# Kernel optimization log

Hardware: AMD Instinct MI355X
Metric: run time of the kernel (lower is better)

Reference implementation:

```python
import jax, jax.numpy as jnp
from jax import lax
import numpy as np

B, C0, C1 = 4, 128, 256
HF = WF = 256
HC = WC = 128
N_CROPS = 2048
WS0, WS1 = 8, 10
PAD0, PAD1 = 0, 1
STRIDE = 8
NW = (WF + 2 * PAD0 - WS0) // STRIDE + 1  # 32 windows per row (same for both crops)


def setup_inputs() -> dict:
    key = jax.random.key(0)
    ks = jax.random.split(key, 16)
    inp = {
        'x0_fine': jax.random.normal(ks[0], (B, C0, HF, WF), jnp.float32),
        'x0_coarse': jax.random.normal(ks[1], (B, C1, HC, WC), jnp.float32),
        'x1_fine': jax.random.normal(ks[2], (B, C0, HF, WF), jnp.float32),
        'x1_coarse': jax.random.normal(ks[3], (B, C1, HC, WC), jnp.float32),
        'proj0_w': jax.random.normal(ks[4], (C1, C0, 1, 1), jnp.float32) * 0.05,
        'proj_last_w': jax.random.normal(ks[5], (C1, C1, 1, 1), jnp.float32) * 0.05,
        'fuse_w1': jax.random.normal(ks[6], (C1, C1, 3, 3), jnp.float32) * 0.02,
        'bn_gamma': jnp.ones((C1,), jnp.float32),
        'bn_beta': jnp.zeros((C1,), jnp.float32),
        'bn_mean': jax.random.normal(ks[7], (C1,), jnp.float32) * 0.1,
        'bn_var': jax.random.uniform(ks[8], (C1,), jnp.float32) + 0.5,
        'fuse_w2': jax.random.normal(ks[9], (C0, C1, 3, 3), jnp.float32) * 0.02,
        'b_idx': jax.random.randint(ks[10], (N_CROPS,), 0, B, jnp.int32),
        'i_idx': jax.random.randint(ks[11], (N_CROPS,), 0, NW * NW, jnp.int32),
        'j_idx': jax.random.randint(ks[12], (N_CROPS,), 0, NW * NW, jnp.int32),
    }
    return inp


def conv2d(x, w, pad):
    return lax.conv_general_dilated(x, w, (1, 1), [(pad, pad), (pad, pad)],
                                    dimension_numbers=('NCHW', 'OIHW', 'NCHW'))


def up2_align_corners(x):
    # bilinear upsample x2 with align_corners=True, separable along H then W
    def interp(x, axis):
        n_in = x.shape[axis]
        n_out = 2 * n_in
        pos = jnp.arange(n_out, dtype=x.dtype) * ((n_in - 1) / (n_out - 1))
        i0 = jnp.clip(jnp.floor(pos).astype(jnp.int32), 0, n_in - 2)
        w = pos - i0.astype(x.dtype)
        a = jnp.take(x, i0, axis=axis)
        b = jnp.take(x, i0 + 1, axis=axis)
        shp = [1] * x.ndim
        shp[axis] = n_out
        w = w.reshape(shp)
        return a * (1 - w) + b * w
    return interp(interp(x, 2), 3)


def fuse(fine, coarse, proj0_w, proj_last_w, fuse_w1, bn_gamma, bn_beta, bn_mean, bn_var, fuse_w2):
    x0 = conv2d(coarse, proj_last_w, 0)                 # projs[-1]
    x0 = conv2d(fine, proj0_w, 0) + up2_align_corners(x0)
    y = conv2d(x0, fuse_w1, 1)
    inv = lax.rsqrt(bn_var + 1e-5)
    y = (y - bn_mean[None, :, None, None]) * (bn_gamma * inv)[None, :, None, None] + bn_beta[None, :, None, None]
    y = jnp.where(y >= 0, y, 0.01 * y)                  # LeakyReLU
    return conv2d(y, fuse_w2, 1)


def crop_windows(x, ws, pad, b, idx):
    # direct sparse window gather; avoids materializing the dense unfold tensor
    xp = jnp.pad(x, ((0, 0), (0, 0), (pad, pad), (pad, pad)))
    nW = (x.shape[3] + 2 * pad - ws) // STRIDE + 1
    r0 = (idx // nW) * STRIDE
    c0 = (idx % nW) * STRIDE
    rows = r0[:, None] + jnp.arange(ws)                 # [n, ws]
    cols = c0[:, None] + jnp.arange(ws)                 # [n, ws]
    crops = xp[b[:, None, None], :, rows[:, :, None], cols[:, None, :]]  # [n, ws, ws, C]
    return jnp.transpose(crops, (0, 3, 1, 2))           # [n, C, ws, ws]


def reference(x0_fine, x0_coarse, x1_fine, x1_coarse, proj0_w, proj_last_w,
              fuse_w1, bn_gamma, bn_beta, bn_mean, bn_var, fuse_w2,
              b_idx, i_idx, j_idx):
    # shapes equal -> concat, fuse once, chunk (matches torch branch)
    fine = jnp.concatenate([x0_fine, x1_fine], 0)
    coarse = jnp.concatenate([x0_coarse, x1_coarse], 0)
    y = fuse(fine, coarse, proj0_w, proj_last_w, fuse_w1, bn_gamma, bn_beta, bn_mean, bn_var, fuse_w2)
    x0, x1 = y[:B], y[B:]
    x0_cropped = crop_windows(x0, WS0, PAD0, b_idx, i_idx)
    x1_cropped = crop_windows(x1, WS1, PAD1, b_idx, j_idx)
    return (x0_cropped, x1_cropped)
```

## Files before the change

### kernel.cpp

```cpp
#include <hip/hip_runtime.h>

typedef __attribute__((ext_vector_type(8))) __bf16 bf16x8;
typedef __attribute__((ext_vector_type(4))) float f32x4;
typedef __attribute__((ext_vector_type(16))) float f32x16;

__device__ __forceinline__ unsigned short fbf(float f) {
  union { float f; unsigned u; } x; x.f = f;
  unsigned r = x.u + 0x7fffu + ((x.u >> 16) & 1u);
  return (unsigned short)(r >> 16);
}
__device__ __forceinline__ float bf2f(unsigned short h) {
  union { unsigned u; float f; } x; x.u = ((unsigned)h) << 16;
  return x.f;
}

#define OFF_WPL 0u
#define OFF_WP0 131072u
#define OFF_WT1 196608u
#define OFF_WT2 1376256u
#define OFF_BNS 1966080u
#define OFF_BNB 1967104u
#define OFF_T1  4194304u
#define OFF_X0  (OFF_T1 + 67108864u)
#define OFF_Y   (OFF_X0 + 268435456u)
#define OFF_YF  OFF_T1

__global__ void prep_kernel(const float* __restrict__ pl, const float* __restrict__ p0,
                            const float* __restrict__ w1, const float* __restrict__ w2,
                            const float* __restrict__ gam, const float* __restrict__ bet,
                            const float* __restrict__ mean, const float* __restrict__ var,
                            unsigned short* __restrict__ wpl, unsigned short* __restrict__ wp0,
                            unsigned short* __restrict__ wt1, unsigned short* __restrict__ wt2,
                            float* __restrict__ bns, float* __restrict__ bnb) {
  int t = blockIdx.x * blockDim.x + threadIdx.x;
  int stride = gridDim.x * blockDim.x;
  for (int i = t; i < 65536; i += stride) wpl[i] = fbf(pl[i]);
  for (int i = t; i < 32768; i += stride) wp0[i] = fbf(p0[i]);
  for (int i = t; i < 589824; i += stride) {
    int e = i & 7, l = (i >> 3) & 63, ks = (i >> 9) & 1;
    int cib = (i >> 10) & 7, cb = (i >> 13) & 7, tap = i >> 16;
    int ci = cib * 32 + ks * 16 + (l >> 5) * 8 + e;
    int co = cb * 32 + (l & 31);
    wt1[i] = fbf(w1[(co * 256 + ci) * 9 + tap]);
  }
  for (int i = t; i < 294912; i += stride) {
    int e = i & 7, l = (i >> 3) & 63, ks = (i >> 9) & 1;
    int cib = (i >> 10) & 7, cb = (i >> 13) & 3, tap = i >> 15;
    int ci = cib * 32 + ks * 16 + (l >> 5) * 8 + e;
    int co = cb * 32 + (l & 31);
    wt2[i] = fbf(w2[(co * 256 + ci) * 9 + tap]);
  }
  for (int i = t; i < 256; i += stride) {
    float s = gam[i] * rsqrtf(var[i] + 1e-5f);
    bns[i] = s; bnb[i] = bet[i] - mean[i] * s;
  }
}

template <int K, int HW, int WD, int EPI>
__global__ __launch_bounds__(512) void gemm1x1_kernel(
    const float* __restrict__ srcA, const float* __restrict__ srcB,
    const unsigned short* __restrict__ wmat,
    unsigned short* __restrict__ outp,
    const unsigned short* __restrict__ t1) {
  __shared__ unsigned short in_lds[128 * 32];
  __shared__ unsigned short w_lds[128 * 32];
  const int tid = threadIdx.x;
  const int pix0 = blockIdx.x * 128;
  const int co0 = blockIdx.y * 128;
  const int n = pix0 / HW;
  const int rem = pix0 % HW;
  const int h = rem / WD;
  const int w0 = rem % WD;
  const float* src = (n < 4) ? (srcA + (size_t)n * K * HW) : (srcB + (size_t)(n - 4) * K * HW);
  const float* rowbase = src + (size_t)h * WD + w0;
  const int wv = tid >> 6, lane = tid & 63;
  const int pw = wv >> 1, cw = wv & 1;
  const int l15 = lane & 15, k8 = lane >> 4;
  f32x4 zero = {0.f, 0.f, 0.f, 0.f};
  f32x4 acc[2][4];
#pragma unroll
  for (int i = 0; i < 2; i++)
#pragma unroll
    for (int j = 0; j < 4; j++) acc[i][j] = zero;
  const int sci = tid >> 4;
  const int sps = (tid & 15) * 8;
  const int wrow = tid >> 2, wsg = tid & 3;
  for (int cib = 0; cib < K / 32; ++cib) {
    int ci0 = cib * 32;
    __syncthreads();
    {
      const float* p = rowbase + (size_t)(ci0 + sci) * HW + sps;
      float4 v0 = *(const float4*)p;
      float4 v1 = *(const float4*)(p + 4);
      float vv[8] = {v0.x, v0.y, v0.z, v0.w, v1.x, v1.y, v1.z, v1.w};
#pragma unroll
      for (int i = 0; i < 8; i++) {
        int row = sps + i;
        int g = (sci >> 3) ^ ((row >> 1) & 3);
        in_lds[row * 32 + g * 8 + (sci & 7)] = fbf(vv[i]);
      }
    }
    {
      int4 v = *(const int4*)&wmat[(size_t)(co0 + wrow) * K + ci0 + wsg * 8];
      *(int4*)&w_lds[wrow * 32 + ((wsg ^ ((wrow >> 1) & 3)) << 3)] = v;
    }
    __syncthreads();
    bf16x8 b[4];
#pragma unroll
    for (int nf = 0; nf < 4; nf++) {
      int row = cw * 64 + nf * 16 + l15;
      b[nf] = *(const bf16x8*)&w_lds[row * 32 + ((k8 ^ ((row >> 1) & 3)) << 3)];
    }
#pragma unroll
    for (int mf = 0; mf < 2; mf++) {
      int row = pw * 32 + mf * 16 + l15;
      bf16x8 a = *(const bf16x8*)&in_lds[row * 32 + ((k8 ^ ((row >> 1) & 3)) << 3)];
#pragma unroll
      for (int nf = 0; nf < 4; nf++)
        acc[mf][nf] = __builtin_amdgcn_mfma_f32_16x16x32_bf16(a, b[nf], acc[mf][nf], 0, 0, 0);
    }
  }
  float fh = 0.f; int i0 = 0;
  if (EPI == 1) {
    float ph = (float)h * (127.0f / 255.0f);
    i0 = (int)ph; if (i0 > 126) i0 = 126;
    fh = ph - (float)i0;
  }
#pragma unroll
  for (int mf = 0; mf < 2; mf++) {
#pragma unroll
    for (int nf = 0; nf < 4; nf++) {
      int co = co0 + cw * 64 + nf * 16 + l15;
#pragma unroll
      for (int r = 0; r < 4; r++) {
        int m = pw * 32 + mf * 16 + k8 * 4 + r;
        float v = acc[mf][nf][r];
        if (EPI == 1) {
          int ww = w0 + m;
          float pww = (float)ww * (127.0f / 255.0f);
          int j0 = (int)pww; if (j0 > 126) j0 = 126;
          float fw = pww - (float)j0;
          const unsigned short* tb = t1 + ((size_t)(n * 128 + i0) * 128 + j0) * 256 + co;
          float a00 = bf2f(tb[0]);
          float a01 = bf2f(tb[256]);
          float a10 = bf2f(tb[128 * 256]);
          float a11 = bf2f(tb[128 * 256 + 256]);
          float top = a00 + fw * (a01 - a00);
          float bot = a10 + fw * (a11 - a10);
          v += top + fh * (bot - top);
        }
        outp[(size_t)(pix0 + m) * 256 + co] = fbf(v);
      }
    }
  }
}

template <int COT, int BNRELU>
__global__ __launch_bounds__(256, 2) void conv3x3_kernel(
    const unsigned short* __restrict__ inp,
    const unsigned short* __restrict__ wtr,
    unsigned short* __restrict__ outp,
    const float* __restrict__ bns, const float* __restrict__ bnb) {
  constexpr int WPT = COT / 32;
  __shared__ unsigned short xl[2][6 * 34 * 32];
  const int tid = threadIdx.x;
  const int bx = blockIdx.x;
  const int n = bx >> 9;
  const int h0 = ((bx >> 3) & 63) * 4;
  const int w0 = (bx & 7) * 32;
  const int co0 = blockIdx.y * 128;
  const int lane = tid & 63, cw = tid >> 6;
  const int l31 = lane & 31, lh = lane >> 5;
  const int cb = (co0 >> 5) + cw;

  f32x16 acc[4];
#pragma unroll
  for (int m = 0; m < 4; m++)
#pragma unroll
    for (int r = 0; r < 16; r++) acc[m][r] = 0.f;

#define FRAG_ADDR(tap, ks, cc) ((((size_t)((tap) * WPT + cb) * 8 + (cc)) * 2 + (ks)) * 512 + lane * 8)

  bf16x8 B[3][3][2];
#pragma unroll
  for (int kh = 0; kh < 3; kh++)
#pragma unroll
    for (int kw = 0; kw < 3; kw++)
#pragma unroll
      for (int ks = 0; ks < 2; ks++)
        B[kh][kw][ks] = *(const bf16x8*)&wtr[FRAG_ADDR(kh * 3 + kw, ks, 0)];

  const size_t nbase = (size_t)n * 256 * 256 * 256;
  for (int s = tid; s < 816; s += 256) {
    int p = s >> 2, g = s & 3;
    int row = p / 34, col = p - row * 34;
    int gh = h0 + row - 1, gw = w0 + col - 1;
    int4 v = make_int4(0, 0, 0, 0);
    if ((unsigned)gh < 256u && (unsigned)gw < 256u)
      v = *(const int4*)&inp[nbase + ((size_t)gh * 256 + gw) * 256 + g * 8];
    *(int4*)&xl[0][p * 32 + ((g ^ ((p >> 1) & 3)) << 3)] = v;
  }
  __syncthreads();

  for (int cib = 0; cib < 8; ++cib) {
    const int cin = (cib + 1) & 7;
    int4 vr[4]; bool va[4]; int ldst[4];
    if (cib < 7) {
#pragma unroll
      for (int q = 0; q < 4; ++q) {
        int s = tid + q * 256;
        va[q] = s < 816;
        int p = s >> 2, g = s & 3;
        int row = p / 34, col = p - row * 34;
        int gh = h0 + row - 1, gw = w0 + col - 1;
        ldst[q] = p * 32 + ((g ^ ((p >> 1) & 3)) << 3);
        vr[q] = make_int4(0, 0, 0, 0);
        if (va[q] && (unsigned)gh < 256u && (unsigned)gw < 256u)
          vr[q] = *(const int4*)&inp[nbase + ((size_t)gh * 256 + gw) * 256 + cin * 32 + g * 8];
      }
    }
    const unsigned short* xb = xl[cib & 1];
    __builtin_amdgcn_s_setprio(1);
#pragma unroll
    for (int r = 0; r < 6; ++r) {
#pragma unroll
      for (int kw = 0; kw < 3; ++kw) {
#pragma unroll
        for (int ks = 0; ks < 2; ++ks) {
          int p = r * 34 + l31 + kw;
          int g = ks * 2 + lh;
          bf16x8 a = *(const bf16x8*)&xb[p * 32 + ((g ^ ((p >> 1) & 3)) << 3)];
#pragma unroll
          for (int kh = 0; kh < 3; ++kh) {
            int m = r - kh;
            if (m >= 0 && m < 4)
              acc[m] = __builtin_amdgcn_mfma_f32_32x32x16_bf16(a, B[kh][kw][ks], acc[m], 0, 0, 0);
          }
        }
      }
      if (r >= 3) {
        int kh = r - 3;
#pragma unroll
        for (int kw = 0; kw < 3; ++kw)
#pragma unroll
          for (int ks = 0; ks < 2; ++ks)
            B[kh][kw][ks] = *(const bf16x8*)&wtr[FRAG_ADDR(kh * 3 + kw, ks, cin)];
      }
    }
    __builtin_amdgcn_s_setprio(0);
    if (cib < 7) {
#pragma unroll
      for (int q = 0; q < 4; ++q)
        if (va[q]) *(int4*)&xl[cin & 1][ldst[q]] = vr[q];
      __syncthreads();
    }
  }
#undef FRAG_ADDR

  const int coL = co0 + cw * 32 + l31;
  float s = 1.f, t = 0.f;
  if (BNRELU) { s = bns[coL]; t = bnb[coL]; }
#pragma unroll
  for (int m = 0; m < 4; ++m) {
    int h = h0 + m;
    size_t rowb = (((size_t)(n * 256 + h) * 256) + w0) * COT + coL;
#pragma unroll
    for (int r = 0; r < 16; ++r) {
      int wofs = (r & 3) + 8 * (r >> 2) + 4 * lh;
      float v = acc[m][r];
      if (BNRELU) { v = v * s + t; v = (v >= 0.f) ? v : 0.01f * v; }
      outp[rowb + (size_t)wofs * COT] = fbf(v);
    }
  }
}

template <int WS, int PAD>
__global__ __launch_bounds__(256) void gather_kernel(
    const unsigned short* __restrict__ yf,
    const int* __restrict__ bidx, const int* __restrict__ widx,
    int bofs, float* __restrict__ outp) {
  const int WS2 = WS * WS;
  __shared__ unsigned short tile[WS * WS * 136];
  const int crop = blockIdx.x, tid = threadIdx.x;
  const int b = bidx[crop] + bofs;
  const int idx = widx[crop];
  const int r0 = (idx >> 5) * 8, c0 = (idx & 31) * 8;
  for (int t = tid; t < WS2 * 16; t += 256) {
    int p = t >> 4, sg = t & 15;
    int r = p / WS, cc = p - r * WS;
    int sr = r0 + r - PAD, sc = c0 + cc - PAD;
    int4 v = make_int4(0, 0, 0, 0);
    if ((unsigned)sr < 256u && (unsigned)sc < 256u)
      v = *(const int4*)&yf[(((size_t)(b * 256 + sr) * 256) + sc) * 128 + sg * 8];
    *(int4*)&tile[p * 136 + sg * 8] = v;
  }
  __syncthreads();
  float* dst = outp + (size_t)crop * 128 * WS2;
  for (int o = tid; o < 128 * WS2; o += 256) {
    int c = o / WS2, p = o - c * WS2;
    dst[o] = bf2f(tile[p * 136 + c]);
  }
}

extern "C" void kernel_launch(void* const* d_in, const int* in_sizes, int n_in,
                              void* d_out, int out_size, void* d_ws, size_t ws_size,
                              hipStream_t stream) {
  const float* x0f = (const float*)d_in[0];
  const float* x0c = (const float*)d_in[1];
  const float* x1f = (const float*)d_in[2];
  const float* x1c = (const float*)d_in[3];
  const float* p0w = (const float*)d_in[4];
  const float* plw = (const float*)d_in[5];
  const float* fw1 = (const float*)d_in[6];
  const float* gam = (const float*)d_in[7];
  const float* bet = (const float*)d_in[8];
  const float* men = (const float*)d_in[9];
  const float* var = (const float*)d_in[10];
  const float* fw2 = (const float*)d_in[11];
  const int* b_idx = (const int*)d_in[12];
  const int* i_idx = (const int*)d_in[13];
  const int* j_idx = (const int*)d_in[14];
  (void)in_sizes; (void)n_in; (void)out_size; (void)ws_size;

  char* ws = (char*)d_ws;
  unsigned short* wpl = (unsigned short*)(ws + OFF_WPL);
  unsigned short* wp0 = (unsigned short*)(ws + OFF_WP0);
  unsigned short* wt1 = (unsigned short*)(ws + OFF_WT1);
  unsigned short* wt2 = (unsigned short*)(ws + OFF_WT2);
  float* bns = (float*)(ws + OFF_BNS);
  float* bnb = (float*)(ws + OFF_BNB);
  unsigned short* t1 = (unsigned short*)(ws + OFF_T1);
  unsigned short* x0 = (unsigned short*)(ws + OFF_X0);
  unsigned short* y = (unsigned short*)(ws + OFF_Y);
  unsigned short* yf = (unsigned short*)(ws + OFF_YF);
  float* out0 = (float*)d_out;
  float* out1 = out0 + (size_t)2048 * 128 * 64;

  prep_kernel<<<512, 256, 0, stream>>>(plw, p0w, fw1, fw2, gam, bet, men, var,
                                       wpl, wp0, wt1, wt2, bns, bnb);
  gemm1x1_kernel<256, 16384, 128, 0><<<dim3(1024, 2), 512, 0, stream>>>(x0c, x1c, wpl, t1, nullptr);
  gemm1x1_kernel<128, 65536, 256, 1><<<dim3(4096, 2), 512, 0, stream>>>(x0f, x1f, wp0, x0, t1);
  conv3x3_kernel<256, 1><<<dim3(4096, 2), 256, 0, stream>>>(x0, wt1, y, bns, bnb);
  conv3x3_kernel<128, 0><<<dim3(4096, 1), 256, 0, stream>>>(y, wt2, yf, nullptr, nullptr);
  gather_kernel<8, 0><<<2048, 256, 0, stream>>>(yf, b_idx, i_idx, 0, out0);
  gather_kernel<10, 1><<<2048, 256, 0, stream>>>(yf, b_idx, j_idx, 4, out1);
}
```

Baseline: 1.234 ms.

## Use group-major LDS layout and double-buffer A fragments across rows in conv3x3

Changes the shared-memory tile layout from a pixel-major XOR-swizzled layout to a channel-group-major layout, where each 8-channel group is stored contiguously across the 204 pixels. The A fragments for the next row are prefetched from LDS into registers while the current row's MFMAs issue. The goal is to simplify address arithmetic, get conflict-free contiguous LDS reads, and hide LDS latency behind the matrix ops. The cost is extra VGPRs for the double-buffered fragments, which may hurt occupancy under launch_bounds(256,2).

New measurement: 1.216 ms. Within noise of the previous version (-1.4%).

```diff
diff --git a/kernel.cpp b/kernel.cpp
--- a/kernel.cpp
+++ b/kernel.cpp
@@ -162,7 +162,7 @@
     unsigned short* __restrict__ outp,
     const float* __restrict__ bns, const float* __restrict__ bnb) {
   constexpr int WPT = COT / 32;
-  __shared__ unsigned short xl[2][6 * 34 * 32];
+  __shared__ unsigned short xl[2][4 * 204 * 8];
   const int tid = threadIdx.x;
   const int bx = blockIdx.x;
   const int n = bx >> 9;
@@ -198,7 +198,7 @@
     int4 v = make_int4(0, 0, 0, 0);
     if ((unsigned)gh < 256u && (unsigned)gw < 256u)
       v = *(const int4*)&inp[nbase + ((size_t)gh * 256 + gw) * 256 + g * 8];
-    *(int4*)&xl[0][p * 32 + ((g ^ ((p >> 1) & 3)) << 3)] = v;
+    *(int4*)&xl[0][(g * 204 + p) * 8] = v;
   }
   __syncthreads();
 
@@ -213,31 +213,42 @@
         int p = s >> 2, g = s & 3;
         int row = p / 34, col = p - row * 34;
         int gh = h0 + row - 1, gw = w0 + col - 1;
-        ldst[q] = p * 32 + ((g ^ ((p >> 1) & 3)) << 3);
+        ldst[q] = (g * 204 + p) * 8;
         vr[q] = make_int4(0, 0, 0, 0);
         if (va[q] && (unsigned)gh < 256u && (unsigned)gw < 256u)
           vr[q] = *(const int4*)&inp[nbase + ((size_t)gh * 256 + gw) * 256 + cin * 32 + g * 8];
       }
     }
     const unsigned short* xb = xl[cib & 1];
+    bf16x8 af[2][6];
+#pragma unroll
+    for (int kw = 0; kw < 3; kw++)
+#pragma unroll
+      for (int ks = 0; ks < 2; ks++)
+        af[0][kw * 2 + ks] = *(const bf16x8*)&xb[((ks * 2 + lh) * 204 + l31 + kw) * 8];
     __builtin_amdgcn_s_setprio(1);
 #pragma unroll
     for (int r = 0; r < 6; ++r) {
-#pragma unroll
-      for (int kw = 0; kw < 3; ++kw) {
-#pragma unroll
-        for (int ks = 0; ks < 2; ++ks) {
-          int p = r * 34 + l31 + kw;
-          int g = ks * 2 + lh;
-          bf16x8 a = *(const bf16x8*)&xb[p * 32 + ((g ^ ((p >> 1) & 3)) << 3)];
-#pragma unroll
-          for (int kh = 0; kh < 3; ++kh) {
+      const int cur = r & 1, nxt = cur ^ 1;
+      if (r < 5) {
+#pragma unroll
+        for (int kw = 0; kw < 3; kw++)
+#pragma unroll
+          for (int ks = 0; ks < 2; ks++)
+            af[nxt][kw * 2 + ks] =
+                *(const bf16x8*)&xb[((ks * 2 + lh) * 204 + (r + 1) * 34 + l31 + kw) * 8];
+      }
+#pragma unroll
+      for (int kw = 0; kw < 3; kw++)
+#pragma unroll
+        for (int ks = 0; ks < 2; ks++)
+#pragma unroll
+          for (int kh = 0; kh < 3; kh++) {
             int m = r - kh;
             if (m >= 0 && m < 4)
-              acc[m] = __builtin_amdgcn_mfma_f32_32x32x16_bf16(a, B[kh][kw][ks], acc[m], 0, 0, 0);
+              acc[m] = __builtin_amdgcn_mfma_f32_32x32x16_bf16(af[cur][kw * 2 + ks],
+                                                               B[kh][kw][ks], acc[m], 0, 0, 0);
           }
-        }
-      }
       if (r >= 3) {
         int kh = r - 3;
 #pragma unroll
```
